# Kernel optimization log

Measured on AMD Instinct MI355X. Metric: run time of the kernel, lower is better.

## Reference

```python
import jax, jax.numpy as jnp
import numpy as np
import itertools

GH, GW = 3, 3  # 3x3 grid, choose-4 scheme -> C(9,4)=126 slots


def _build_9c4_masks(H, W, gh=GH, gw=GW):
    hs = [int(round(i * H / gh)) for i in range(gh + 1)]
    ws = [int(round(j * W / gw)) for j in range(gw + 1)]
    rects = [(hs[i], hs[i + 1], ws[j], ws[j + 1])
             for i in range(gh) for j in range(gw)]
    masks = []
    for comb in itertools.combinations(range(len(rects)), 4):
        m = np.zeros((H, W), dtype=np.float32)
        for idx in comb:
            y0, y1, x0, x1 = rects[idx]
            m[y0:y1, x0:x1] = 1.0
        m = m / max(m.sum(), 1.0)
        masks.append(m)
    return np.stack(masks, axis=0)  # (S=126, H, W)


def setup_inputs() -> dict:
    key = jax.random.key(0)
    B, D, H, W = 256, 512, 28, 28
    feats = jax.random.normal(key, (B, D, H, W), dtype=jnp.float32)
    masks = jnp.asarray(_build_9c4_masks(H, W))  # fixed buffer, (126, H, W)
    return {"feats": feats, "masks": masks}


def reference(feats, masks):
    # (feats[:,None] * masks[None,:,None]).sum((-1,-2)) expressed as a
    # batched contraction over the spatial dims -> (B, S, D)
    return jnp.einsum('bdhw,shw->bsd', feats, masks)
```

## Files before the change

kernel.cpp:

```cpp
#include <hip/hip_runtime.h>


#define BLOCK 256
#define G     16
#define GC    8
#define F4C   (GC * 196)
#define NS    126
#define NR    9

__global__ void slots_kernel(
    const float* __restrict__ feats,
    const float* __restrict__ masks,
    float* __restrict__ out)
{
    __shared__ float4 buf[F4C];
    __shared__ float  rs[G * 28 * 3];
    __shared__ float  rect_t[NR * G];
    __shared__ float  wtab[NS * NR];

    const int t        = threadIdx.x;
    const int img_base = blockIdx.x * G;
    const int b        = img_base >> 9;
    const int d0       = img_base & 511;

    for (int i = t; i < NS * NR; i += BLOCK) {
        const int s  = i / NR;
        const int r  = i - s * NR;
        const int bi = r / 3, bj = r - bi * 3;
        const int yc = (bi == 0) ? 4 : ((bi == 1) ? 14 : 23);
        const int xc = (bj == 0) ? 4 : ((bj == 1) ? 14 : 23);
        wtab[i] = masks[s * 784 + yc * 28 + xc];
    }

    for (int c = 0; c < 2; ++c) {
        const float4* src = reinterpret_cast<const float4*>(feats)
                          + (size_t)(img_base + c * GC) * 196;
        #pragma unroll
        for (int k = 0; k < 6; ++k)
            buf[t + k * 256] = src[t + k * 256];
        if (t < 32)
            buf[t + 1536] = src[t + 1536];
        __syncthreads();

        if (t < GC * 28) {
            const float4* p = &buf[t * 7];
            float4 v0 = p[0], v1 = p[1], v2 = p[2], v3 = p[3],
                   v4 = p[4], v5 = p[5], v6 = p[6];
            float s0 = v0.x + v0.y + v0.z + v0.w + v1.x + v1.y + v1.z + v1.w + v2.x;
            float s1 = v2.y + v2.z + v2.w + v3.x + v3.y + v3.z + v3.w + v4.x + v4.y + v4.z;
            float s2 = v4.w + v5.x + v5.y + v5.z + v5.w + v6.x + v6.y + v6.z + v6.w;
            const int R = c * 224 + t;
            rs[R * 3 + 0] = s0;
            rs[R * 3 + 1] = s1;
            rs[R * 3 + 2] = s2;
        }
        __syncthreads();
    }

    if (t < G * NR) {
        const int g  = t / NR, r = t - g * NR;
        const int bi = r / 3, bj = r - bi * 3;
        const int h0 = (bi == 0) ? 0 : ((bi == 1) ? 9 : 19);
        const int h1 = (bi == 0) ? 9 : ((bi == 1) ? 19 : 28);
        float a = 0.f;
        for (int h = h0; h < h1; ++h)
            a += rs[(g * 28 + h) * 3 + bj];
        rect_t[r * G + g] = a;
    }
    __syncthreads();

    float* outb = out + (size_t)b * NS * 512 + d0;
    for (int i = t; i < (NS * G) / 4; i += BLOCK) {
        const int s  = i >> 2;
        const int c4 = (i & 3) * 4;
        const float* wp = &wtab[s * NR];
        float4 a; a.x = a.y = a.z = a.w = 0.f;
        #pragma unroll
        for (int r = 0; r < NR; ++r) {
            const float  w  = wp[r];
            const float4 rv = *reinterpret_cast<const float4*>(&rect_t[r * G + c4]);
            a.x += w * rv.x; a.y += w * rv.y; a.z += w * rv.z; a.w += w * rv.w;
        }
        *reinterpret_cast<float4*>(&outb[(size_t)s * 512 + c4]) = a;
    }
}

extern "C" void kernel_launch(void* const* d_in, const int* in_sizes, int n_in,
                              void* d_out, int out_size, void* d_ws, size_t ws_size,
                              hipStream_t stream) {
    const float* feats = (const float*)d_in[0];
    const float* masks = (const float*)d_in[1];
    float* out = (float*)d_out;

    const int blocks = (256 * 512) / G;
    slots_kernel<<<blocks, BLOCK, 0, stream>>>(feats, masks, out);
}
```

Before: 106.6 us.

## Double-buffer feature chunks with async global-to-LDS loads and larger image groups

Each block now handles 64 feature maps instead of 16, working through them in 8-map chunks. The next chunk is streamed straight into LDS with global_load_lds into a second buffer while the current chunk is reduced, and one barrier per chunk replaces two. The larger group also spreads the mask-table setup over more work and writes 64 contiguous floats per slot row. The cost is more LDS per block, held to 2 blocks per SM via launch bounds, and 4x fewer blocks, which may reduce latency hiding.

```diff
diff --git a/kernel.cpp b/kernel.cpp
--- a/kernel.cpp
+++ b/kernel.cpp
@@ -2,18 +2,25 @@
 
 
 #define BLOCK 256
-#define G     16
+#define G     64
 #define GC    8
+#define NCH   (G / GC)
 #define F4C   (GC * 196)
 #define NS    126
 #define NR    9
 
-__global__ void slots_kernel(
+__device__ __forceinline__ void gload_lds16(const float4* g, float4* l) {
+    __builtin_amdgcn_global_load_lds(
+        (const __attribute__((address_space(1))) void*)g,
+        (__attribute__((address_space(3))) void*)l, 16, 0, 0);
+}
+
+__global__ __launch_bounds__(BLOCK, 2) void slots_kernel(
     const float* __restrict__ feats,
     const float* __restrict__ masks,
     float* __restrict__ out)
 {
-    __shared__ float4 buf[F4C];
+    __shared__ float4 buf[2][F4C];
     __shared__ float  rs[G * 28 * 3];
     __shared__ float  rect_t[NR * G];
     __shared__ float  wtab[NS * NR];
@@ -23,6 +30,18 @@
     const int b        = img_base >> 9;
     const int d0       = img_base & 511;
 
+    const float4* fbase = reinterpret_cast<const float4*>(feats)
+                        + (size_t)img_base * 196;
+    const int wbase = t & ~63;
+
+    {
+        const float4* src = fbase;
+        #pragma unroll
+        for (int k = 0; k < 6; ++k)
+            gload_lds16(src + k * 256 + t, &buf[0][k * 256 + wbase]);
+        if (t < 32)
+            gload_lds16(src + 1536 + t, &buf[0][1536]);
+    }
     for (int i = t; i < NS * NR; i += BLOCK) {
         const int s  = i / NR;
         const int r  = i - s * NR;
@@ -32,18 +51,19 @@
         wtab[i] = masks[s * 784 + yc * 28 + xc];
     }
 
-    for (int c = 0; c < 2; ++c) {
-        const float4* src = reinterpret_cast<const float4*>(feats)
-                          + (size_t)(img_base + c * GC) * 196;
-        #pragma unroll
-        for (int k = 0; k < 6; ++k)
-            buf[t + k * 256] = src[t + k * 256];
-        if (t < 32)
-            buf[t + 1536] = src[t + 1536];
+    for (int c = 0; c < NCH; ++c) {
         __syncthreads();
-
+        if (c + 1 < NCH) {
+            const float4* src = fbase + (size_t)(c + 1) * F4C;
+            float4* dst = buf[(c + 1) & 1];
+            #pragma unroll
+            for (int k = 0; k < 6; ++k)
+                gload_lds16(src + k * 256 + t, dst + k * 256 + wbase);
+            if (t < 32)
+                gload_lds16(src + 1536 + t, dst + 1536);
+        }
         if (t < GC * 28) {
-            const float4* p = &buf[t * 7];
+            const float4* p = &buf[c & 1][t * 7];
             float4 v0 = p[0], v1 = p[1], v2 = p[2], v3 = p[3],
                    v4 = p[4], v5 = p[5], v6 = p[6];
             float s0 = v0.x + v0.y + v0.z + v0.w + v1.x + v1.y + v1.z + v1.w + v2.x;
@@ -54,11 +74,11 @@
             rs[R * 3 + 1] = s1;
             rs[R * 3 + 2] = s2;
         }
-        __syncthreads();
     }
+    __syncthreads();
 
-    if (t < G * NR) {
-        const int g  = t / NR, r = t - g * NR;
+    for (int i = t; i < G * NR; i += BLOCK) {
+        const int g  = i / NR, r = i - (i / NR) * NR;
         const int bi = r / 3, bj = r - bi * 3;
         const int h0 = (bi == 0) ? 0 : ((bi == 1) ? 9 : 19);
         const int h1 = (bi == 0) ? 9 : ((bi == 1) ? 19 : 28);
@@ -71,8 +91,8 @@
 
     float* outb = out + (size_t)b * NS * 512 + d0;
     for (int i = t; i < (NS * G) / 4; i += BLOCK) {
-        const int s  = i >> 2;
-        const int c4 = (i & 3) * 4;
+        const int s  = i >> 4;
+        const int c4 = (i & 15) << 2;
         const float* wp = &wtab[s * NR];
         float4 a; a.x = a.y = a.z = a.w = 0.f;
         #pragma unroll
```

New measurement: 105.1 us. Within noise of the previous version (-1.4%).
